# Kernel optimization log

Hardware: AMD Instinct MI355X
Metric: run time of the kernel (lower is better)

## Reference

```python
import jax, jax.numpy as jnp
import numpy as np

B, TIN, SOUT = 128, 256, 32
IN_DIM, H, L = 512, 512, 2
OUT_DIM = 100
D3 = 3 * OUT_DIM          # decoder effective out_dim (gt_type == 'tmc')
CAT = D3 + H              # 812, input dim of attn linears


def setup_inputs() -> dict:
    key = jax.random.key(0)
    ks = jax.random.split(key, 20)
    g = lambda k, s: jax.random.normal(k, s, dtype=jnp.float32) * 0.02
    return {
        "x": jax.random.normal(ks[0], (B, TIN, IN_DIM), dtype=jnp.float32),
        "target": jax.random.normal(ks[1], (B, SOUT + 1, OUT_DIM, 3), dtype=jnp.float32),
        # encoder GRU (num_layers=2, layer inputs are both 512-dim so weights stack)
        "enc_Wih": g(ks[2], (L, 3 * H, IN_DIM)),
        "enc_Whh": g(ks[3], (L, 3 * H, H)),
        "enc_bih": g(ks[4], (L, 3 * H)),
        "enc_bhh": g(ks[5], (L, 3 * H)),
        # decoder GRU (layer0 input = D3=300, layer1 input = H=512)
        "dec_Wih0": g(ks[6], (3 * H, D3)),
        "dec_Wih1": g(ks[7], (3 * H, H)),
        "dec_Whh": g(ks[8], (L, 3 * H, H)),
        "dec_bih": g(ks[9], (L, 3 * H)),
        "dec_bhh": g(ks[10], (L, 3 * H)),
        # attention linears
        "attnW_w": g(ks[11], (TIN, CAT)), "attnW_b": g(ks[12], (TIN,)),
        "attnC_w": g(ks[13], (D3, CAT)), "attnC_b": g(ks[14], (D3,)),
        # output MLP
        "out1_w": g(ks[15], (D3, H)), "out1_b": g(ks[16], (D3,)),
        "out2_w": g(ks[17], (D3, D3)), "out2_b": g(ks[18], (D3,)),
    }


def gru_cell(x, h, Wih, Whh, bih, bhh):
    """PyTorch-convention GRU cell. x:(B,Din) h:(B,H) -> (B,H)."""
    gi = x @ Wih.T + bih
    gh = h @ Whh.T + bhh
    ir, iz, inn = jnp.split(gi, 3, axis=-1)
    hr, hz, hn = jnp.split(gh, 3, axis=-1)
    r = jax.nn.sigmoid(ir + hr)
    z = jax.nn.sigmoid(iz + hz)
    n = jnp.tanh(inn + r * hn)
    return (1.0 - z) * n + z * h


def reference(x, target, enc_Wih, enc_Whh, enc_bih, enc_bhh,
              dec_Wih0, dec_Wih1, dec_Whh, dec_bih, dec_bhh,
              attnW_w, attnW_b, attnC_w, attnC_b,
              out1_w, out1_b, out2_w, out2_b):
    # ---- encoder: 2-layer GRU over time, zero initial hidden ----
    seq = jnp.transpose(x, (1, 0, 2))  # (T, B, D)
    hs = []
    for l in range(L):
        def step(h, xt, l=l):
            h2 = gru_cell(xt, h, enc_Wih[l], enc_Whh[l], enc_bih[l], enc_bhh[l])
            return h2, h2
        hT, seq = jax.lax.scan(step, jnp.zeros((B, H), x.dtype), seq)
        hs.append(hT)
    enc_out = jnp.transpose(seq, (1, 0, 2))      # (B, TIN, H)
    enc_hidden = jnp.stack(hs)                   # (L, B, H)

    # ---- decoder with teacher forcing (teacher_forcing_ratio=1.0) ----
    tgt = target[..., :3].reshape(B, SOUT + 1, D3)   # (B, SOUT+1, 300)
    xs = jnp.transpose(tgt[:, :SOUT, :], (1, 0, 2))  # (SOUT, B, 300)

    def dec_step(hidden, xt):
        cat = jnp.concatenate([xt, hidden[-1]], axis=-1)          # (B, 812)
        aw = jax.nn.softmax(cat @ attnW_w.T + attnW_b, axis=-1)   # (B, TIN)
        wctx = jnp.einsum('bt,bth->bh', aw, enc_out)              # (B, H)
        xc = jax.nn.relu(jnp.concatenate([xt, wctx], axis=-1) @ attnC_w.T + attnC_b)  # (B, 300)
        h0 = gru_cell(xc, hidden[0], dec_Wih0, dec_Whh[0], dec_bih[0], dec_bhh[0])
        h1 = gru_cell(h0, hidden[1], dec_Wih1, dec_Whh[1], dec_bih[1], dec_bhh[1])
        o = (h1 @ out1_w.T + out1_b) @ out2_w.T + out2_b          # (B, 300)
        return jnp.stack([h0, h1]), (o, aw)

    dec_hidden, (outs, aws) = jax.lax.scan(dec_step, enc_hidden, xs)
    dec_out = jnp.transpose(outs, (1, 0, 2))       # (B, SOUT, 300)
    attn_weights = jnp.transpose(aws, (1, 0, 2))   # (B, SOUT, TIN)
    return dec_out, dec_hidden, attn_weights
```

## Files before the change

kernel.cpp:

```cpp
#include <hip/hip_runtime.h>
#include <hip/hip_bf16.h>
#include <math.h>


#define NWG 128
#define TPB 256

typedef unsigned short u16;
typedef unsigned int   u32;
typedef short v8s __attribute__((ext_vector_type(8)));
typedef float v4f __attribute__((ext_vector_type(4)));

#define MFMA_(a,b,c) __builtin_amdgcn_mfma_f32_16x16x32_bf16((a),(b),(c),0,0,0)

__device__ __forceinline__ u16 f2bf(float f){
  unsigned u = __builtin_bit_cast(unsigned, f);
  unsigned r = u + 0x7FFFu + ((u >> 16) & 1u);
  return (u16)(r >> 16);
}
__device__ __forceinline__ float bf2f(u16 s){
  unsigned u = ((unsigned)s) << 16;
  return __builtin_bit_cast(float, u);
}
__device__ __forceinline__ void splitstore(u16* ph, u16* pl, float v){
  u16 h = f2bf(v); ph[0] = h; pl[0] = f2bf(v - bf2f(h));
}
__device__ __forceinline__ float sigm(float x){ return 1.f / (1.f + __expf(-x)); }
__device__ __forceinline__ float tanh_f(float x){
  float ax = fabsf(x);
  float t = __expf(-2.f * ax);
  float r = (1.f - t) / (1.f + t);
  return copysignf(r, x);
}

__device__ __forceinline__ v8s ldfrag(const u16* base, size_t ld, int r0, int k0){
  int lane = threadIdx.x & 63;
  const u16* p = base + (size_t)(r0 + (lane & 15)) * ld + (size_t)(k0 + ((lane >> 4) << 3));
  return *(const v8s*)p;
}

__device__ __forceinline__ void ldx4x4_sc0(v8s&o0,v8s&o1,v8s&o2,v8s&o3,
    const u16*p0,const u16*p1,const u16*p2,const u16*p3){
  asm volatile(
    "global_load_dwordx4 %0, %4, off sc0\n\t"
    "global_load_dwordx4 %1, %5, off sc0\n\t"
    "global_load_dwordx4 %2, %6, off sc0\n\t"
    "global_load_dwordx4 %3, %7, off sc0\n\t"
    "s_waitcnt vmcnt(0)"
    : "=&v"(o0),"=&v"(o1),"=&v"(o2),"=&v"(o3)
    : "v"(p0),"v"(p1),"v"(p2),"v"(p3) : "memory");
}
__device__ __forceinline__ void ldus4_sc0(u32&o0,u32&o1,u32&o2,u32&o3,
    const u16*p0,const u16*p1,const u16*p2,const u16*p3){
  asm volatile(
    "global_load_ushort %0, %4, off sc0\n\t"
    "global_load_ushort %1, %5, off sc0\n\t"
    "global_load_ushort %2, %6, off sc0\n\t"
    "global_load_ushort %3, %7, off sc0\n\t"
    "s_waitcnt vmcnt(0)"
    : "=&v"(o0),"=&v"(o1),"=&v"(o2),"=&v"(o3)
    : "v"(p0),"v"(p1),"v"(p2),"v"(p3) : "memory");
}

__device__ __forceinline__ v8s ldfrag_w(const u16* wlds, int gate, int kt){
  int lane = threadIdx.x & 63;
  int rr = lane & 15;
  int ch = (kt*4 + (lane >> 4)) ^ (rr & 7);
  return *(const v8s*)(wlds + (size_t)((gate*16 + rr)*64 + ch) * 8);
}
__device__ void stage_wslice(const float* Wf, u16* wlds, int col0){
  for (int idx = threadIdx.x; idx < 3*16*64; idx += TPB){
    int ch = idx & 63, rr = (idx >> 6) & 15, g = idx >> 10;
    const float* src = Wf + ((size_t)(g*512 + col0 + rr))*512 + ch*8;
    v4f f0 = *(const v4f*)src, f1 = *(const v4f*)(src + 4);
    v8s o;
    #pragma unroll
    for (int j=0;j<4;j++){ o[j] = (short)f2bf(f0[j]); o[4+j] = (short)f2bf(f1[j]); }
    *(v8s*)(wlds + (size_t)((g*16 + rr)*64 + (ch ^ (rr & 7))) * 8) = o;
  }
}
__device__ void stage_wslice_u16(const u16* Wh, const u16* Wl, u16* dh, u16* dl, int col0){
  for (int idx = threadIdx.x; idx < 3*16*64; idx += TPB){
    int ch = idx & 63, rr = (idx >> 6) & 15, g = idx >> 10;
    size_t so = ((size_t)(g*512 + col0 + rr))*512 + ch*8;
    size_t o  = (size_t)((g*16 + rr)*64 + (ch ^ (rr & 7))) * 8;
    *(v8s*)(dh+o) = *(const v8s*)(Wh+so);
    *(v8s*)(dl+o) = *(const v8s*)(Wl+so);
  }
}

struct KArgs {
  const float *x, *target, *eWih_f, *eWhh_f, *ebih, *ebhh;
  const float *dWih0_f, *dWih1_f, *dWhh_f, *dbih, *dbhh;
  const float *aWw_f, *aWb, *aCw_f, *aCb, *o1w_f, *o1b, *o2w_f, *o2b;
  float* out;
  u32 *flags, *genp, *ecnt, *lctr;
  u16 *ebf, *ehh;
  u16 *xhi, *h0hi, *h1hi, *encout;
  u16 *dWih0h,*dWih0l,*dWih1h,*dWih1l,*dWhhh,*dWhhl;
  u16 *Wwhh,*Wwhl,*Wwxh,*Wwxl,*Wchh,*Wchl,*Wcxh,*Wcxl;
  u16 *o2wh,*o2wl,*o1Th,*o1Tl,*Wph,*Wpl;
  float *bpr;
  u16 *xth,*xtl;
  float *preW,*preC;
  u16 *dh0h,*dh0l,*dh1h,*dh1l;
  float *logits;
  u16 *wcth,*wctl,*xch,*xcl;
};

__device__ __forceinline__ u32 ldcp(const u32* p){
  u32 r;
  asm volatile("global_load_dword %0, %1, off sc0 sc1\n\ts_waitcnt vmcnt(0)"
               : "=&v"(r) : "v"(p) : "memory");
  return r;
}

__device__ void gbar(u32* flags, u32* genp, u32 target){
  __syncthreads();
  int wg = blockIdx.x, tid = threadIdx.x;
  if (wg == 0){
    if (tid > 0 && tid < NWG){
      while (ldcp(&flags[tid]) < target) __builtin_amdgcn_s_sleep(1);
    }
    __syncthreads();
    if (tid == 0)
      __hip_atomic_fetch_add(genp, 1u, __ATOMIC_RELEASE, __HIP_MEMORY_SCOPE_AGENT);
  } else {
    if (tid == 0){
      __hip_atomic_fetch_add(&flags[wg], 1u, __ATOMIC_RELEASE, __HIP_MEMORY_SCOPE_AGENT);
      while (ldcp(genp) < target) __builtin_amdgcn_s_sleep(1);
    }
  }
  __builtin_amdgcn_fence(__ATOMIC_ACQUIRE, "agent");
  __syncthreads();
}

__device__ void lbar(u32* ctr, u32 target){
  __syncthreads();
  if (threadIdx.x == 0){
    __hip_atomic_fetch_add(ctr, 1u, __ATOMIC_RELAXED, __HIP_MEMORY_SCOPE_AGENT);
    while (ldcp(ctr) < target) __builtin_amdgcn_s_sleep(1);
  }
  __syncthreads();
}

__device__ __forceinline__ v4f tile_xwT(const u16* Ah, const u16* Al, size_t lda, int nks,
                                        const u16* Bh, const u16* Bl, size_t ldb,
                                        int row0, int brow0, v4f* red){
  int tid = threadIdx.x, w = tid >> 6, lane = tid & 63;
  v4f acc[4];
  #pragma unroll
  for (int i=0;i<4;i++) acc[i] = (v4f){0.f,0.f,0.f,0.f};
  for (int ks = w; ks < nks; ks += 4){
    int k0 = ks * 32;
    v8s bh = ldfrag(Bh, ldb, brow0, k0);
    v8s bl = ldfrag(Bl, ldb, brow0, k0);
    #pragma unroll
    for (int rt=0; rt<4; rt++){
      v8s a  = ldfrag(Ah, lda, row0 + rt*16, k0);
      v8s al = ldfrag(Al, lda, row0 + rt*16, k0);
      acc[rt] = MFMA_(a,  bh, acc[rt]);
      acc[rt] = MFMA_(al, bh, acc[rt]);
      acc[rt] = MFMA_(a,  bl, acc[rt]);
    }
  }
  __syncthreads();
  red[(0*4+w)*64+lane]=acc[0]; red[(1*4+w)*64+lane]=acc[1];
  red[(2*4+w)*64+lane]=acc[2]; red[(3*4+w)*64+lane]=acc[3];
  __syncthreads();
  v4f g = red[(w*4+0)*64+lane];
  g += red[(w*4+1)*64+lane]; g += red[(w*4+2)*64+lane]; g += red[(w*4+3)*64+lane];
  return g;
}

__device__ __forceinline__ void gru_tile_pin(const u16* Axh, const u16* Axl, size_t ldx, int nkx,
                                             const u16* Ahh, const u16* Ahl,
                                             const u16* Wi,  const u16* Wil, size_t ldwi,
                                             const u16* whp, const u16* wlp,
                                             int row0, int col0, v4f* red, v4f* gate){
  int tid = threadIdx.x, w = tid >> 6, lane = tid & 63;
  v4f acc[4][4];
  #pragma unroll
  for (int i=0;i<4;i++){
    #pragma unroll
    for (int j=0;j<4;j++) acc[i][j] = (v4f){0.f,0.f,0.f,0.f};
  }
  for (int ks = w; ks < nkx; ks += 4){
    int k0 = ks * 32;
    v8s br = ldfrag(Wi, ldwi,        col0, k0);
    v8s bz = ldfrag(Wi, ldwi,  512 + col0, k0);
    v8s bn = ldfrag(Wi, ldwi, 1024 + col0, k0);
    v8s brl = ldfrag(Wil, ldwi, col0, k0);
    v8s bzl = ldfrag(Wil, ldwi, 512+col0, k0);
    v8s bnl = ldfrag(Wil, ldwi, 1024+col0, k0);
    #pragma unroll
    for (int rt=0; rt<4; rt++){
      v8s a  = ldfrag(Axh, ldx, row0 + rt*16, k0);
      v8s al = ldfrag(Axl, ldx, row0 + rt*16, k0);
      acc[rt][0] = MFMA_(a, br, acc[rt][0]); acc[rt][0] = MFMA_(al, br, acc[rt][0]); acc[rt][0] = MFMA_(a, brl, acc[rt][0]);
      acc[rt][1] = MFMA_(a, bz, acc[rt][1]); acc[rt][1] = MFMA_(al, bz, acc[rt][1]); acc[rt][1] = MFMA_(a, bzl, acc[rt][1]);
      acc[rt][2] = MFMA_(a, bn, acc[rt][2]); acc[rt][2] = MFMA_(al, bn, acc[rt][2]); acc[rt][2] = MFMA_(a, bnl, acc[rt][2]);
    }
  }
  for (int ks = w; ks < 16; ks += 4){
    int k0 = ks * 32;
    v8s br  = ldfrag_w(whp, 0, ks), bz  = ldfrag_w(whp, 1, ks), bn  = ldfrag_w(whp, 2, ks);
    v8s brl = ldfrag_w(wlp, 0, ks), bzl = ldfrag_w(wlp, 1, ks), bnl = ldfrag_w(wlp, 2, ks);
    #pragma unroll
    for (int rt=0; rt<4; rt++){
      v8s a  = ldfrag(Ahh, 512, row0 + rt*16, k0);
      v8s al = ldfrag(Ahl, 512, row0 + rt*16, k0);
      acc[rt][0] = MFMA_(a, br, acc[rt][0]); acc[rt][0] = MFMA_(al, br, acc[rt][0]); acc[rt][0] = MFMA_(a, brl, acc[rt][0]);
      acc[rt][1] = MFMA_(a, bz, acc[rt][1]); acc[rt][1] = MFMA_(al, bz, acc[rt][1]); acc[rt][1] = MFMA_(a, bzl, acc[rt][1]);
      acc[rt][3] = MFMA_(a, bn, acc[rt][3]); acc[rt][3] = MFMA_(al, bn, acc[rt][3]); acc[rt][3] = MFMA_(a, bnl, acc[rt][3]);
    }
  }
  #pragma unroll
  for (int ty=0; ty<4; ty++){
    __syncthreads();
    red[(0*4+w)*64+lane]=acc[0][ty]; red[(1*4+w)*64+lane]=acc[1][ty];
    red[(2*4+w)*64+lane]=acc[2][ty]; red[(3*4+w)*64+lane]=acc[3][ty];
    __syncthreads();
    v4f g = red[(w*4+0)*64+lane];
    g += red[(w*4+1)*64+lane]; g += red[(w*4+2)*64+lane]; g += red[(w*4+3)*64+lane];
    gate[ty] = g;
  }
}

__device__ __forceinline__ void gru_combine(const v4f* gate, const float* bih, const float* bhh,
                                            const u16* Hph, const u16* Hpl,
                                            u16* Hnh, u16* Hnl,
                                            int row0, int col0){
  int tid = threadIdx.x, w = tid >> 6, lane = tid & 63;
  int col  = col0 + (lane & 15);
  int rowb = row0 + w*16 + ((lane >> 4) << 2);
  float bir = bih[col], biz = bih[512+col], bin = bih[1024+col];
  float bhr = bhh[col], bhz = bhh[512+col], bhn = bhh[1024+col];
  #pragma unroll
  for (int e=0; e<4; e++){
    int row = rowb + e;
    float r = sigm(gate[0][e] + bir + bhr);
    float z = sigm(gate[1][e] + biz + bhz);
    float n = tanh_f(gate[2][e] + bin + r * (gate[3][e] + bhn));
    float hp = bf2f(Hph[(size_t)row*512 + col]) + bf2f(Hpl[(size_t)row*512 + col]);
    float hv = (1.f - z) * n + z * hp;
    splitstore(&Hnh[(size_t)row*512+col], &Hnl[(size_t)row*512+col], hv);
  }
}

__device__ void enc_step3(const u16* Xb, size_t ldX, const u16* Hp, u16* Hn,
                          u16* encw, int t, const u16* wI, const u16* wH,
                          const float* bih, const float* bhh, int col0, int row0){
  const int tid = threadIdx.x, w = tid>>6, lane = tid&63;
  v4f aR=(v4f){0,0,0,0}, aZ=aR, aNI=aR, aNH=aR;
  const int r0 = row0 + w*16;
  for (int kt=0; kt<16; ++kt){
    int k0 = kt*32;
    v8s bi0=ldfrag_w(wI,0,kt), bi1=ldfrag_w(wI,1,kt), bi2=ldfrag_w(wI,2,kt);
    v8s bh0=ldfrag_w(wH,0,kt), bh1=ldfrag_w(wH,1,kt), bh2=ldfrag_w(wH,2,kt);
    v8s ax = ldfrag(Xb, ldX, r0, k0);
    v8s ah = ldfrag(Hp, 512, r0, k0);
    aR=MFMA_(ax,bi0,aR); aZ=MFMA_(ax,bi1,aZ); aNI=MFMA_(ax,bi2,aNI);
    aR=MFMA_(ah,bh0,aR); aZ=MFMA_(ah,bh1,aZ); aNH=MFMA_(ah,bh2,aNH);
  }
  int col = col0 + (lane&15);
  float bir=bih[col], biz=bih[512+col], bin=bih[1024+col];
  float bhr=bhh[col], bhz=bhh[512+col], bhn=bhh[1024+col];
  int rowb = r0 + ((lane>>4)<<2);
  #pragma unroll
  for (int e=0;e<4;e++){
    int row = rowb + e;
    float r = sigm(aR[e] + bir + bhr);
    float z = sigm(aZ[e] + biz + bhz);
    float n = tanh_f(aNI[e] + bin + r*(aNH[e] + bhn));
    float hp = bf2f(Hp[(size_t)row*512 + col]);
    float hv = (1.f-z)*n + z*hp;
    u16 h16 = f2bf(hv);
    Hn[(size_t)row*512 + col] = h16;
    if (encw) encw[((size_t)row*256 + t)*512 + col] = h16;
  }
}

__device__ void enc_stepL(const u16* Xb, size_t ldX, int xsc0,
                          const u16* Hp, u16* Hn, u16* encw, int t,
                          const u16* Wih, const u16* Whh,
                          const float* bih, const float* bhh,
                          int b0, int c0, v4f* red){
  const int tid = threadIdx.x, w = tid>>6, lane = tid&63;
  v4f acc[2][4];
  #pragma unroll
  for (int i=0;i<2;i++)
    #pragma unroll
    for (int j=0;j<4;j++) acc[i][j] = (v4f){0,0,0,0};
  const size_t lo = (size_t)((lane>>4)<<3);
  v8s ax0,ax1,ax2,ax3, ah0,ah1,ah2,ah3;
  {
    const u16* hrow = Hp + (size_t)(b0 + (lane&15))*512 + lo;
    ldx4x4_sc0(ah0,ah1,ah2,ah3,
               hrow + (w*4+0)*32, hrow + (w*4+1)*32, hrow + (w*4+2)*32, hrow + (w*4+3)*32);
  }
  if (xsc0){
    const u16* xrow = Xb + (size_t)(lane&15)*ldX + lo;
    ldx4x4_sc0(ax0,ax1,ax2,ax3,
               xrow + (w*4+0)*32, xrow + (w*4+1)*32, xrow + (w*4+2)*32, xrow + (w*4+3)*32);
  } else {
    ax0 = ldfrag(Xb, ldX, 0, (w*4+0)*32);
    ax1 = ldfrag(Xb, ldX, 0, (w*4+1)*32);
    ax2 = ldfrag(Xb, ldX, 0, (w*4+2)*32);
    ax3 = ldfrag(Xb, ldX, 0, (w*4+3)*32);
  }
  v8s axs[4] = {ax0,ax1,ax2,ax3};
  v8s ahs[4] = {ah0,ah1,ah2,ah3};
  #pragma unroll
  for (int j=0;j<4;j++){
    int k0 = (w*4+j)*32;
    #pragma unroll
    for (int ct=0; ct<2; ct++){
      int cc = c0 + ct*16;
      acc[ct][0] = MFMA_(axs[j], ldfrag(Wih,512,cc,k0),      acc[ct][0]);
      acc[ct][1] = MFMA_(axs[j], ldfrag(Wih,512,512+cc,k0),  acc[ct][1]);
      acc[ct][2] = MFMA_(axs[j], ldfrag(Wih,512,1024+cc,k0), acc[ct][2]);
      acc[ct][0] = MFMA_(ahs[j], ldfrag(Whh,512,cc,k0),      acc[ct][0]);
      acc[ct][1] = MFMA_(ahs[j], ldfrag(Whh,512,512+cc,k0),  acc[ct][1]);
      acc[ct][3] = MFMA_(ahs[j], ldfrag(Whh,512,1024+cc,k0), acc[ct][3]);
    }
  }
  __syncthreads();
  #pragma unroll
  for (int ct=0; ct<2; ct++)
    #pragma unroll
    for (int g=0; g<4; g++)
      red[((ct*4+g)*4 + w)*64 + lane] = acc[ct][g];
  __syncthreads();
  if (w < 2){
    v4f gate[4];
    #pragma unroll
    for (int g=0; g<4; g++){
      v4f s = red[((w*4+g)*4+0)*64+lane];
      s += red[((w*4+g)*4+1)*64+lane];
      s += red[((w*4+g)*4+2)*64+lane];
      s += red[((w*4+g)*4+3)*64+lane];
      gate[g] = s;
    }
    int col = c0 + w*16 + (lane&15);
    int lb  = ((lane>>4)<<2);
    u32 hp0,hp1,hp2,hp3;
    ldus4_sc0(hp0,hp1,hp2,hp3,
              Hp + (size_t)(b0+lb+0)*512 + col, Hp + (size_t)(b0+lb+1)*512 + col,
              Hp + (size_t)(b0+lb+2)*512 + col, Hp + (size_t)(b0+lb+3)*512 + col);
    u32 hpv[4] = {hp0,hp1,hp2,hp3};
    float bir=bih[col], biz=bih[512+col], bin=bih[1024+col];
    float bhr=bhh[col], bhz=bhh[512+col], bhn=bhh[1024+col];
    #pragma unroll
    for (int e=0;e<4;e++){
      int row = b0 + lb + e;
      float r = sigm(gate[0][e] + bir + bhr);
      float z = sigm(gate[1][e] + biz + bhz);
      float n = tanh_f(gate[2][e] + bin + r*(gate[3][e] + bhn));
      float hv = (1.f-z)*n + z*bf2f((u16)hpv[e]);
      u16 h16 = f2bf(hv);
      Hn[(size_t)row*512 + col] = h16;
      if (encw) encw[((size_t)row*256 + t)*512 + col] = h16;
    }
  }
}

__device__ __forceinline__ float blk_max(float v, float* sred){
  #pragma unroll
  for (int off=32; off>0; off>>=1) v = fmaxf(v, __shfl_xor(v, off, 64));
  __syncthreads();
  if ((threadIdx.x & 63) == 0) sred[threadIdx.x >> 6] = v;
  __syncthreads();
  return fmaxf(fmaxf(sred[0], sred[1]), fmaxf(sred[2], sred[3]));
}
__device__ __forceinline__ float blk_sum(float v, float* sred){
  #pragma unroll
  for (int off=32; off>0; off>>=1) v += __shfl_xor(v, off, 64);
  __syncthreads();
  if ((threadIdx.x & 63) == 0) sred[threadIdx.x >> 6] = v;
  __syncthreads();
  return sred[0] + sred[1] + sred[2] + sred[3];
}

#define DECOUT_OFF 0
#define DECHID_OFF 1228800
#define ATTN_OFF   1359872

__global__ void __launch_bounds__(TPB, 1) traffic_kernel(KArgs A){
  __shared__ struct { u16 wI[3*16*64*8]; u16 wH[3*16*64*8]; } WL;
  __shared__ v4f red[8*4*64];
  __shared__ float sred[4];
  __shared__ float awl2[256];
  __shared__ int sh_xcd, sh_slot, sh_bal;
  const int tid = threadIdx.x;
  const int wg  = blockIdx.x;
  const size_t gtid = (size_t)wg * TPB + tid;
  const size_t P = (size_t)NWG * TPB;
  u32 bt = 0;

  {
    u32 xcd;
    asm volatile("s_getreg_b32 %0, hwreg(HW_REG_XCC_ID)" : "=s"(xcd));
    if (tid == 0){
      sh_xcd = (int)(xcd & 7);
      sh_slot = (int)__hip_atomic_fetch_add(&A.ecnt[sh_xcd], 1u, __ATOMIC_RELAXED, __HIP_MEMORY_SCOPE_AGENT);
    }
    __syncthreads();
  }

  for (size_t i=gtid; i<128UL*256*512; i+=P) A.xhi[i] = f2bf(A.x[i]);
  for (size_t i=gtid; i<2UL*1536*512; i+=P){ A.ebf[i]=f2bf(A.eWih_f[i]); A.ehh[i]=f2bf(A.eWhh_f[i]); }
  for (size_t i=gtid; i<1536UL*320; i+=P){
    size_t r=i/320, c=i%320;
    float v = (c<300)? A.dWih0_f[r*300+c] : 0.f;
    splitstore(&A.dWih0h[i], &A.dWih0l[i], v);
  }
  for (size_t i=gtid; i<1536UL*512; i+=P) splitstore(&A.dWih1h[i], &A.dWih1l[i], A.dWih1_f[i]);
  for (size_t i=gtid; i<2UL*1536*512; i+=P) splitstore(&A.dWhhh[i], &A.dWhhl[i], A.dWhh_f[i]);
  for (size_t i=gtid; i<256UL*512; i+=P){ size_t r=i>>9, c=i&511; splitstore(&A.Wwhh[i], &A.Wwhl[i], A.aWw_f[r*812+300+c]); }
  for (size_t i=gtid; i<256UL*320; i+=P){ size_t r=i/320, c=i%320; float v=(c<300)? A.aWw_f[r*812+c]:0.f; splitstore(&A.Wwxh[i], &A.Wwxl[i], v); }
  for (size_t i=gtid; i<304UL*512; i+=P){ size_t r=i>>9, c=i&511; float v=(r<300)? A.aCw_f[r*812+300+c]:0.f; splitstore(&A.Wchh[i], &A.Wchl[i], v); }
  for (size_t i=gtid; i<304UL*320; i+=P){ size_t r=i/320, c=i%320; float v=(r<300&&c<300)? A.aCw_f[r*812+c]:0.f; splitstore(&A.Wcxh[i], &A.Wcxl[i], v); }
  for (size_t i=gtid; i<320UL*320; i+=P){ size_t r=i/320, c=i%320; float v=(r<300&&c<300)? A.o2w_f[r*300+c]:0.f; splitstore(&A.o2wh[i], &A.o2wl[i], v); }
  for (size_t i=gtid; i<512UL*320; i+=P){
    size_t j=i/320, k=i%320;
    float v = (k<300)? A.o1w_f[k*512+j] : 0.f;
    splitstore(&A.o1Th[i], &A.o1Tl[i], v);
  }
  for (size_t i=gtid; i<304; i+=P){
    float s = 0.f;
    if (i < 300){
      s = A.o2b[i];
      const float* wrow = A.o2w_f + i*300;
      for (int k=0;k<300;k++) s += wrow[k] * A.o1b[k];
    }
    A.bpr[i] = s;
  }
  for (size_t i=gtid; i<32UL*128*320; i+=P){
    size_t sb=i/320, c=i%320, s2=sb>>7, b=sb&127;
    float v = (c<300)? A.target[(b*33+s2)*300 + c] : 0.f;
    splitstore(&A.xth[i], &A.xtl[i], v);
  }
  for (size_t i=gtid; i<65536; i+=P){ A.h0hi[i]=0; A.h1hi[i]=0; }
  for (size_t i=gtid; i<128UL*320; i+=P){ A.xch[i]=0; A.xcl[i]=0; }
  gbar(A.flags, A.genp, ++bt);

  if (tid == 0){
    int ok = 1;
    for (int x2=0; x2<8; x2++)
      ok &= (__hip_atomic_fetch_add(&A.ecnt[x2], 0u, __ATOMIC_RELAXED, __HIP_MEMORY_SCOPE_AGENT) == 16u);
    sh_bal = ok;
  }
  __syncthreads();
  const int vwg = sh_bal ? (sh_xcd*16 + sh_slot) : wg;

  for (int tl = vwg; tl < 1024; tl += NWG){
    int rb = tl >> 4, cb = tl & 15;
    int row0 = rb*64, col0 = cb*16;
    v4f g = tile_xwT(A.xth, A.xtl, 320, 10, A.Wwxh, A.Wwxl, 320, row0, col0, red);
    int w = tid>>6, lane = tid&63;
    int col = col0 + (lane&15), rowb = row0 + w*16 + ((lane>>4)<<2);
    #pragma unroll
    for (int e=0;e<4;e++){ int row=rowb+e; A.preW[(size_t)row*256+col] = g[e] + A.aWb[col]; }
  }
  for (int tl = vwg; tl < 1216; tl += NWG){
    int rb = tl / 19, cb = tl % 19;
    int row0 = rb*64, col0 = cb*16;
    v4f g = tile_xwT(A.xth, A.xtl, 320, 10, A.Wcxh, A.Wcxl, 320, row0, col0, red);
    int w = tid>>6, lane = tid&63;
    int col = col0 + (lane&15), rowb = row0 + w*16 + ((lane>>4)<<2);
    #pragma unroll
    for (int e=0;e<4;e++){
      int row=rowb+e;
      float v = (col<300)? (g[e] + A.aCb[col]) : 0.f;
      A.preC[(size_t)row*320+col] = v;
    }
  }
  for (int tl = vwg; tl < 160; tl += NWG){
    int rt = tl >> 5, ct = tl & 31;
    int row0 = rt*64, col0 = ct*16;
    v4f g = tile_xwT(A.o2wh, A.o2wl, 320, 10, A.o1Th, A.o1Tl, 320, row0, col0, red);
    int w = tid>>6, lane = tid&63;
    int col = col0 + (lane&15), rowb = row0 + w*16 + ((lane>>4)<<2);
    #pragma unroll
    for (int e=0;e<4;e++){
      int row = rowb+e;
      if (row < 304) splitstore(&A.Wph[(size_t)row*512+col], &A.Wpl[(size_t)row*512+col], g[e]);
    }
  }
  gbar(A.flags, A.genp, ++bt);

  if (sh_bal){
    const int b0 = sh_xcd*16, c0 = sh_slot*32;
    u32* ctr = A.lctr + sh_xcd*16;
    u32 lt = 0;
    for (int t=0; t<256; ++t){
      enc_stepL(A.xhi + (size_t)b0*131072 + (size_t)t*512, 131072, 0,
                A.h0hi + (size_t)t*65536, A.h0hi + (size_t)(t+1)*65536,
                nullptr, 0, A.ebf, A.ehh, A.ebih, A.ebhh, b0, c0, red);
      lbar(ctr, 16u*(++lt));
    }
    const u16* W1i = A.ebf + (size_t)1536*512;
    const u16* W1h = A.ehh + (size_t)1536*512;
    for (int t=0; t<256; ++t){
      enc_stepL(A.h0hi + (size_t)(t+1)*65536 + (size_t)b0*512, 512, 1,
                A.h1hi + (size_t)(t&1)*65536, A.h1hi + (size_t)((t+1)&1)*65536,
                A.encout, t, W1i, W1h, A.ebih + 1536, A.ebhh + 1536, b0, c0, red);
      lbar(ctr, 16u*(++lt));
    }
  } else {
    const int grp  = vwg >> 6;
    const int half = (vwg >> 5) & 1;
    const int col0 = (vwg & 31) * 16;
    const int row0 = half * 64;
    stage_wslice(A.eWih_f + (size_t)grp*1536*512, WL.wI, col0);
    stage_wslice(A.eWhh_f + (size_t)grp*1536*512, WL.wH, col0);
    __syncthreads();
    const float* bih = A.ebih + grp*1536;
    const float* bhh = A.ebhh + grp*1536;
    for (int k=0; k<=256; ++k){
      if (grp == 0){
        if (k < 256)
          enc_step3(A.xhi + (size_t)k*512, (size_t)256*512,
                    A.h0hi + (size_t)k*65536, A.h0hi + (size_t)(k+1)*65536,
                    nullptr, 0, WL.wI, WL.wH, bih, bhh, col0, row0);
      } else {
        if (k >= 1){
          int t = k-1;
          enc_step3(A.h0hi + (size_t)k*65536, 512,
                    A.h1hi + (size_t)(t&1)*65536, A.h1hi + (size_t)((t+1)&1)*65536,
                    A.encout, t, WL.wI, WL.wH, bih, bhh, col0, row0);
        }
      }
      gbar(A.flags, A.genp, ++bt);
    }
  }
  gbar(A.flags, A.genp, ++bt);

  for (size_t i=gtid; i<65536; i+=P){
    A.dh0h[i] = A.h0hi[(size_t)256*65536 + i]; A.dh0l[i] = 0;
    A.dh1h[i] = A.h1hi[i];                     A.dh1l[i] = 0;
  }
  if (vwg < 64){
    int cb = vwg & 31;
    stage_wslice_u16(A.dWhhh, A.dWhhl, WL.wI, WL.wH, cb*16);
  } else {
    int cb = (vwg - 64) & 31;
    stage_wslice_u16(A.dWhhh + (size_t)1536*512, A.dWhhl + (size_t)1536*512, WL.wI, WL.wH, cb*16);
  }
  gbar(A.flags, A.genp, ++bt);

  for (int s=0; s<32; s++){
    const u16* h0ph = A.dh0h + (size_t)(s&1)*65536;
    const u16* h0pl = A.dh0l + (size_t)(s&1)*65536;
    u16* h0nh = A.dh0h + (size_t)((s+1)&1)*65536;
    u16* h0nl = A.dh0l + (size_t)((s+1)&1)*65536;
    const u16* h1ph = A.dh1h + (size_t)(s&1)*65536;
    const u16* h1pl = A.dh1l + (size_t)(s&1)*65536;
    u16* h1nh = A.dh1h + (size_t)((s+1)&1)*65536;
    u16* h1nl = A.dh1l + (size_t)((s+1)&1)*65536;

    if (vwg < 32){
      int rb = vwg >> 4, cb = vwg & 15;
      int row0 = rb*64, col0 = cb*16;
      v4f g = tile_xwT(h1ph, h1pl, 512, 16, A.Wwhh, A.Wwhl, 512, row0, col0, red);
      const float* pre = A.preW + (size_t)s*128*256;
      int w = tid>>6, lane = tid&63;
      int col = col0 + (lane&15), rowb = row0 + w*16 + ((lane>>4)<<2);
      #pragma unroll
      for (int e=0;e<4;e++){ int row=rowb+e; A.logits[(size_t)row*256+col] = g[e] + pre[(size_t)row*256+col]; }
    } else if (vwg >= 64 && vwg < 102 && s > 0){
      int v2 = vwg - 64;
      int rb = v2 / 19, cb = v2 % 19;
      int row0 = rb*64, col0 = cb*16;
      v4f g = tile_xwT(h1ph, h1pl, 512, 16, A.Wph, A.Wpl, 512, row0, col0, red);
      int w = tid>>6, lane = tid&63;
      int col = col0 + (lane&15), rowb = row0 + w*16 + ((lane>>4)<<2);
      #pragma unroll
      for (int e=0;e<4;e++){
        int row = rowb+e;
        if (col < 300) A.out[DECOUT_OFF + ((size_t)row*32 + (s-1))*300 + col] = g[e] + A.bpr[col];
      }
    }
    gbar(A.flags, A.genp, ++bt);

    {
      int b = vwg;
      float v = A.logits[(size_t)b*256 + tid];
      float m = blk_max(v, sred);
      float e = __expf(v - m);
      float ssum = blk_sum(e, sred);
      float awv = e / ssum;
      awl2[tid] = awv;
      A.out[ATTN_OFF + ((size_t)b*32 + s)*256 + tid] = awv;
      __syncthreads();
      int w4 = tid >> 6, lane = tid & 63;
      const u16* ebase = A.encout + (size_t)b*256*512 + (size_t)(w4*64)*512 + lane*8;
      float acc8[8];
      #pragma unroll
      for (int q=0;q<8;q++) acc8[q]=0.f;
      for (int j=0;j<64;++j){
        float wv = awl2[w4*64+j];
        v8s ev = *(const v8s*)(ebase + (size_t)j*512);
        #pragma unroll
        for (int q=0;q<8;q++) acc8[q] += wv * bf2f((u16)ev[q]);
      }
      float* rr = (float*)red;
      #pragma unroll
      for (int q=0;q<8;q++) rr[(size_t)tid*8+q] = acc8[q];
      __syncthreads();
      #pragma unroll
      for (int cc=0; cc<2; ++cc){
        int col = tid*2+cc;
        float sum = 0.f;
        #pragma unroll
        for (int w2=0; w2<4; ++w2) sum += rr[(((size_t)w2*64 + (col>>3))<<3) + (col&7)];
        splitstore(&A.wcth[(size_t)b*512+col], &A.wctl[(size_t)b*512+col], sum);
      }
    }
    gbar(A.flags, A.genp, ++bt);

    if (vwg < 38){
      int rb = vwg / 19, cb = vwg % 19;
      int row0 = rb*64, col0 = cb*16;
      v4f g = tile_xwT(A.wcth, A.wctl, 512, 16, A.Wchh, A.Wchl, 512, row0, col0, red);
      const float* pre = A.preC + (size_t)s*128*320;
      int w = tid>>6, lane = tid&63;
      int col = col0 + (lane&15), rowb = row0 + w*16 + ((lane>>4)<<2);
      #pragma unroll
      for (int e=0;e<4;e++){
        int row = rowb+e;
        float v = (col<300)? fmaxf(g[e] + pre[(size_t)row*320+col], 0.f) : 0.f;
        splitstore(&A.xch[(size_t)row*320+col], &A.xcl[(size_t)row*320+col], v);
      }
    }
    gbar(A.flags, A.genp, ++bt);

    if (vwg < 64){
      int rb = vwg >> 5, cb = vwg & 31;
      int row0 = rb*64, col0 = cb*16;
      v4f gate[4];
      gru_tile_pin(A.xch, A.xcl, 320, 10, h0ph, h0pl,
                   A.dWih0h, A.dWih0l, 320, WL.wI, WL.wH, row0, col0, red, gate);
      gru_combine(gate, A.dbih, A.dbhh, h0ph, h0pl, h0nh, h0nl, row0, col0);
    }
    gbar(A.flags, A.genp, ++bt);

    if (vwg >= 64){
      int v2 = vwg - 64;
      int rb = v2 >> 5, cb = v2 & 31;
      int row0 = rb*64, col0 = cb*16;
      v4f gate[4];
      gru_tile_pin(h0nh, h0nl, 512, 16, h1ph, h1pl,
                   A.dWih1h, A.dWih1l, 512, WL.wI, WL.wH, row0, col0, red, gate);
      gru_combine(gate, A.dbih + 1536, A.dbhh + 1536, h1ph, h1pl, h1nh, h1nl, row0, col0);
    }
    gbar(A.flags, A.genp, ++bt);
  }

  if (vwg >= 64 && vwg < 102){
    int v2 = vwg - 64;
    int rb = v2 / 19, cb = v2 % 19;
    int row0 = rb*64, col0 = cb*16;
    v4f g = tile_xwT(A.dh1h, A.dh1l, 512, 16, A.Wph, A.Wpl, 512, row0, col0, red);
    int w = tid>>6, lane = tid&63;
    int col = col0 + (lane&15), rowb = row0 + w*16 + ((lane>>4)<<2);
    #pragma unroll
    for (int e=0;e<4;e++){
      int row = rowb+e;
      if (col < 300) A.out[DECOUT_OFF + ((size_t)row*32 + 31)*300 + col] = g[e] + A.bpr[col];
    }
  }

  for (size_t i=gtid; i<65536; i+=P){
    A.out[DECHID_OFF + i]         = bf2f(A.dh0h[i]) + bf2f(A.dh0l[i]);
    A.out[DECHID_OFF + 65536 + i] = bf2f(A.dh1h[i]) + bf2f(A.dh1l[i]);
  }
}

extern "C" void kernel_launch(void* const* d_in, const int* in_sizes, int n_in,
                              void* d_out, int out_size, void* d_ws, size_t ws_size,
                              hipStream_t stream){
  (void)in_sizes; (void)n_in; (void)out_size; (void)ws_size;
  KArgs A;
  A.x       = (const float*)d_in[0];  A.target = (const float*)d_in[1];
  A.eWih_f  = (const float*)d_in[2];  A.eWhh_f = (const float*)d_in[3];
  A.ebih    = (const float*)d_in[4];  A.ebhh   = (const float*)d_in[5];
  A.dWih0_f = (const float*)d_in[6];  A.dWih1_f= (const float*)d_in[7];
  A.dWhh_f  = (const float*)d_in[8];  A.dbih   = (const float*)d_in[9];
  A.dbhh    = (const float*)d_in[10];
  A.aWw_f   = (const float*)d_in[11]; A.aWb    = (const float*)d_in[12];
  A.aCw_f   = (const float*)d_in[13]; A.aCb    = (const float*)d_in[14];
  A.o1w_f   = (const float*)d_in[15]; A.o1b    = (const float*)d_in[16];
  A.o2w_f   = (const float*)d_in[17]; A.o2b    = (const float*)d_in[18];
  A.out = (float*)d_out;

  char* w = (char*)d_ws;
  size_t off = 0;
  auto alloc = [&](size_t bytes)->char*{
    char* p = w + off; off += (bytes + 255) & ~(size_t)255; return p;
  };
  char* barp = alloc(4096);
  A.flags  = (u32*)barp;
  A.genp   = (u32*)(barp + 2048);
  A.ecnt   = (u32*)(barp + 2304);
  A.lctr   = (u32*)(barp + 2560);
  A.ebf    = (u16*)alloc(2UL*1536*512*2);
  A.ehh    = (u16*)alloc(2UL*1536*512*2);
  A.xhi    = (u16*)alloc(128UL*256*512*2);
  A.h0hi   = (u16*)alloc(257UL*128*512*2);
  A.h1hi   = (u16*)alloc(2UL*128*512*2);
  A.encout = A.xhi;
  A.dWih0h = (u16*)alloc(1536UL*320*2); A.dWih0l = (u16*)alloc(1536UL*320*2);
  A.dWih1h = (u16*)alloc(1536UL*512*2); A.dWih1l = (u16*)alloc(1536UL*512*2);
  A.dWhhh  = (u16*)alloc(2UL*1536*512*2); A.dWhhl = (u16*)alloc(2UL*1536*512*2);
  A.Wwhh   = (u16*)alloc(256UL*512*2);  A.Wwhl   = (u16*)alloc(256UL*512*2);
  A.Wwxh   = (u16*)alloc(256UL*320*2);  A.Wwxl   = (u16*)alloc(256UL*320*2);
  A.Wchh   = (u16*)alloc(304UL*512*2);  A.Wchl   = (u16*)alloc(304UL*512*2);
  A.Wcxh   = (u16*)alloc(304UL*320*2);  A.Wcxl   = (u16*)alloc(304UL*320*2);
  A.o2wh   = (u16*)alloc(320UL*320*2);  A.o2wl   = (u16*)alloc(320UL*320*2);
  A.o1Th   = (u16*)alloc(512UL*320*2);  A.o1Tl   = (u16*)alloc(512UL*320*2);
  A.Wph    = (u16*)alloc(304UL*512*2);  A.Wpl    = (u16*)alloc(304UL*512*2);
  A.bpr    = (float*)alloc(304UL*4);
  A.xth    = (u16*)alloc(32UL*128*320*2); A.xtl  = (u16*)alloc(32UL*128*320*2);
  A.preW   = (float*)alloc(32UL*128*256*4);
  A.preC   = (float*)alloc(32UL*128*320*4);
  A.dh0h   = (u16*)alloc(2UL*65536*2); A.dh0l = (u16*)alloc(2UL*65536*2);
  A.dh1h   = (u16*)alloc(2UL*65536*2); A.dh1l = (u16*)alloc(2UL*65536*2);
  A.logits = (float*)alloc(128UL*256*4);
  A.wcth   = (u16*)alloc(128UL*512*2); A.wctl = (u16*)alloc(128UL*512*2);
  A.xch    = (u16*)alloc(128UL*320*2); A.xcl  = (u16*)alloc(128UL*320*2);

  hipMemsetAsync(d_ws, 0, 4096, stream);
  traffic_kernel<<<dim3(NWG), dim3(TPB), 0, stream>>>(A);
}
```

Measured before the change: 7.792 ms.

## Replace atomic barriers with padded flag-store barriers and XCD-local L2 polling

```diff
diff --git a/kernel.cpp b/kernel.cpp
--- a/kernel.cpp
+++ b/kernel.cpp
@@ -94,7 +94,7 @@
   const float *dWih0_f, *dWih1_f, *dWhh_f, *dbih, *dbhh;
   const float *aWw_f, *aWb, *aCw_f, *aCb, *o1w_f, *o1b, *o2w_f, *o2b;
   float* out;
-  u32 *flags, *genp, *ecnt, *lctr;
+  u32 *flags, *genp, *ecnt, *lflags, *lgen;
   u16 *ebf, *ehh;
   u16 *xhi, *h0hi, *h1hi, *encout;
   u16 *dWih0h,*dWih0l,*dWih1h,*dWih1l,*dWhhh,*dWhhl;
@@ -114,20 +114,36 @@
                : "=&v"(r) : "v"(p) : "memory");
   return r;
 }
-
-__device__ void gbar(u32* flags, u32* genp, u32 target){
-  __syncthreads();
+__device__ __forceinline__ void stcp(u32* p, u32 v){
+  asm volatile("global_store_dword %0, %1, off sc0 sc1" :: "v"(p), "v"(v) : "memory");
+}
+__device__ __forceinline__ u32 ldl(const u32* p, u32 it){
+  u32 r;
+  if ((it & 63u) != 0u)
+    asm volatile("global_load_dword %0, %1, off sc0\n\ts_waitcnt vmcnt(0)"
+                 : "=&v"(r) : "v"(p) : "memory");
+  else
+    asm volatile("global_load_dword %0, %1, off sc0 sc1\n\ts_waitcnt vmcnt(0)"
+                 : "=&v"(r) : "v"(p) : "memory");
+  return r;
+}
+__device__ __forceinline__ void stl(u32* p, u32 v){
+  asm volatile("global_store_dword %0, %1, off sc0" :: "v"(p), "v"(v) : "memory");
+}
+
+__device__ void gbarF(u32* flags, u32* genp, u32 target){
+  __syncthreads();
+  __builtin_amdgcn_fence(__ATOMIC_RELEASE, "agent");
   int wg = blockIdx.x, tid = threadIdx.x;
   if (wg == 0){
     if (tid > 0 && tid < NWG){
-      while (ldcp(&flags[tid]) < target) __builtin_amdgcn_s_sleep(1);
+      while (ldcp(flags + (size_t)tid*16) < target) __builtin_amdgcn_s_sleep(1);
     }
     __syncthreads();
-    if (tid == 0)
-      __hip_atomic_fetch_add(genp, 1u, __ATOMIC_RELEASE, __HIP_MEMORY_SCOPE_AGENT);
+    if (tid == 0) stcp(genp, target);
   } else {
     if (tid == 0){
-      __hip_atomic_fetch_add(&flags[wg], 1u, __ATOMIC_RELEASE, __HIP_MEMORY_SCOPE_AGENT);
+      stcp(flags + (size_t)wg*16, target);
       while (ldcp(genp) < target) __builtin_amdgcn_s_sleep(1);
     }
   }
@@ -135,11 +151,23 @@
   __syncthreads();
 }
 
-__device__ void lbar(u32* ctr, u32 target){
-  __syncthreads();
-  if (threadIdx.x == 0){
-    __hip_atomic_fetch_add(ctr, 1u, __ATOMIC_RELAXED, __HIP_MEMORY_SCOPE_AGENT);
-    while (ldcp(ctr) < target) __builtin_amdgcn_s_sleep(1);
+__device__ void lbarF(u32* lflags, u32* lgen, int slot, u32 target){
+  asm volatile("s_waitcnt vmcnt(0)" ::: "memory");
+  __syncthreads();
+  int tid = threadIdx.x;
+  if (slot == 0){
+    if (tid >= 1 && tid < 16){
+      u32 it = 0;
+      while (ldl(lflags + (size_t)tid*16, ++it) < target) __builtin_amdgcn_s_sleep(1);
+    }
+    __syncthreads();
+    if (tid == 0) stl(lgen, target);
+  } else {
+    if (tid == 0){
+      stl(lflags + (size_t)slot*16, target);
+      u32 it = 0;
+      while (ldl(lgen, ++it) < target) __builtin_amdgcn_s_sleep(1);
+    }
   }
   __syncthreads();
 }
@@ -403,7 +431,8 @@
     asm volatile("s_getreg_b32 %0, hwreg(HW_REG_XCC_ID)" : "=s"(xcd));
     if (tid == 0){
       sh_xcd = (int)(xcd & 7);
-      sh_slot = (int)__hip_atomic_fetch_add(&A.ecnt[sh_xcd], 1u, __ATOMIC_RELAXED, __HIP_MEMORY_SCOPE_AGENT);
+      sh_slot = (int)__hip_atomic_fetch_add(A.ecnt + (size_t)(xcd & 7)*16, 1u,
+                                            __ATOMIC_RELAXED, __HIP_MEMORY_SCOPE_AGENT);
     }
     __syncthreads();
   }
@@ -443,12 +472,12 @@
   }
   for (size_t i=gtid; i<65536; i+=P){ A.h0hi[i]=0; A.h1hi[i]=0; }
   for (size_t i=gtid; i<128UL*320; i+=P){ A.xch[i]=0; A.xcl[i]=0; }
-  gbar(A.flags, A.genp, ++bt);
+  gbarF(A.flags, A.genp, ++bt);
 
   if (tid == 0){
     int ok = 1;
     for (int x2=0; x2<8; x2++)
-      ok &= (__hip_atomic_fetch_add(&A.ecnt[x2], 0u, __ATOMIC_RELAXED, __HIP_MEMORY_SCOPE_AGENT) == 16u);
+      ok &= (ldcp(A.ecnt + (size_t)x2*16) == 16u);
     sh_bal = ok;
   }
   __syncthreads();
@@ -488,17 +517,18 @@
       if (row < 304) splitstore(&A.Wph[(size_t)row*512+col], &A.Wpl[(size_t)row*512+col], g[e]);
     }
   }
-  gbar(A.flags, A.genp, ++bt);
+  gbarF(A.flags, A.genp, ++bt);
 
   if (sh_bal){
     const int b0 = sh_xcd*16, c0 = sh_slot*32;
-    u32* ctr = A.lctr + sh_xcd*16;
+    u32* lfl = A.lflags + (size_t)sh_xcd*256;
+    u32* lgn = A.lgen   + (size_t)sh_xcd*16;
     u32 lt = 0;
     for (int t=0; t<256; ++t){
       enc_stepL(A.xhi + (size_t)b0*131072 + (size_t)t*512, 131072, 0,
                 A.h0hi + (size_t)t*65536, A.h0hi + (size_t)(t+1)*65536,
                 nullptr, 0, A.ebf, A.ehh, A.ebih, A.ebhh, b0, c0, red);
-      lbar(ctr, 16u*(++lt));
+      lbarF(lfl, lgn, sh_slot, ++lt);
     }
     const u16* W1i = A.ebf + (size_t)1536*512;
     const u16* W1h = A.ehh + (size_t)1536*512;
@@ -506,7 +536,7 @@
       enc_stepL(A.h0hi + (size_t)(t+1)*65536 + (size_t)b0*512, 512, 1,
                 A.h1hi + (size_t)(t&1)*65536, A.h1hi + (size_t)((t+1)&1)*65536,
                 A.encout, t, W1i, W1h, A.ebih + 1536, A.ebhh + 1536, b0, c0, red);
-      lbar(ctr, 16u*(++lt));
+      lbarF(lfl, lgn, sh_slot, ++lt);
     }
   } else {
     const int grp  = vwg >> 6;
@@ -532,10 +562,10 @@
                     A.encout, t, WL.wI, WL.wH, bih, bhh, col0, row0);
         }
       }
-      gbar(A.flags, A.genp, ++bt);
-    }
-  }
-  gbar(A.flags, A.genp, ++bt);
+      gbarF(A.flags, A.genp, ++bt);
+    }
+  }
+  gbarF(A.flags, A.genp, ++bt);
 
   for (size_t i=gtid; i<65536; i+=P){
     A.dh0h[i] = A.h0hi[(size_t)256*65536 + i]; A.dh0l[i] = 0;
@@ -548,7 +578,7 @@
     int cb = (vwg - 64) & 31;
     stage_wslice_u16(A.dWhhh + (size_t)1536*512, A.dWhhl + (size_t)1536*512, WL.wI, WL.wH, cb*16);
   }
-  gbar(A.flags, A.genp, ++bt);
+  gbarF(A.flags, A.genp, ++bt);
 
   for (int s=0; s<32; s++){
     const u16* h0ph = A.dh0h + (size_t)(s&1)*65536;
@@ -582,7 +612,7 @@
         if (col < 300) A.out[DECOUT_OFF + ((size_t)row*32 + (s-1))*300 + col] = g[e] + A.bpr[col];
       }
     }
-    gbar(A.flags, A.genp, ++bt);
+    gbarF(A.flags, A.genp, ++bt);
 
     {
       int b = vwg;
@@ -618,7 +648,7 @@
         splitstore(&A.wcth[(size_t)b*512+col], &A.wctl[(size_t)b*512+col], sum);
       }
     }
-    gbar(A.flags, A.genp, ++bt);
+    gbarF(A.flags, A.genp, ++bt);
 
     if (vwg < 38){
       int rb = vwg / 19, cb = vwg % 19;
@@ -634,7 +664,7 @@
         splitstore(&A.xch[(size_t)row*320+col], &A.xcl[(size_t)row*320+col], v);
       }
     }
-    gbar(A.flags, A.genp, ++bt);
+    gbarF(A.flags, A.genp, ++bt);
 
     if (vwg < 64){
       int rb = vwg >> 5, cb = vwg & 31;
@@ -644,7 +674,7 @@
                    A.dWih0h, A.dWih0l, 320, WL.wI, WL.wH, row0, col0, red, gate);
       gru_combine(gate, A.dbih, A.dbhh, h0ph, h0pl, h0nh, h0nl, row0, col0);
     }
-    gbar(A.flags, A.genp, ++bt);
+    gbarF(A.flags, A.genp, ++bt);
 
     if (vwg >= 64){
       int v2 = vwg - 64;
@@ -655,7 +685,7 @@
                    A.dWih1h, A.dWih1l, 512, WL.wI, WL.wH, row0, col0, red, gate);
       gru_combine(gate, A.dbih + 1536, A.dbhh + 1536, h1ph, h1pl, h1nh, h1nl, row0, col0);
     }
-    gbar(A.flags, A.genp, ++bt);
+    gbarF(A.flags, A.genp, ++bt);
   }
 
   if (vwg >= 64 && vwg < 102){
@@ -700,11 +730,12 @@
   auto alloc = [&](size_t bytes)->char*{
     char* p = w + off; off += (bytes + 255) & ~(size_t)255; return p;
   };
-  char* barp = alloc(4096);
+  char* barp = alloc(32768);
   A.flags  = (u32*)barp;
-  A.genp   = (u32*)(barp + 2048);
-  A.ecnt   = (u32*)(barp + 2304);
-  A.lctr   = (u32*)(barp + 2560);
+  A.genp   = (u32*)(barp + 8192);
+  A.ecnt   = (u32*)(barp + 8448);
+  A.lflags = (u32*)(barp + 9472);
+  A.lgen   = (u32*)(barp + 17664);
   A.ebf    = (u16*)alloc(2UL*1536*512*2);
   A.ehh    = (u16*)alloc(2UL*1536*512*2);
   A.xhi    = (u16*)alloc(128UL*256*512*2);
@@ -731,6 +762,6 @@
   A.wcth   = (u16*)alloc(128UL*512*2); A.wctl = (u16*)alloc(128UL*512*2);
   A.xch    = (u16*)alloc(128UL*320*2); A.xcl  = (u16*)alloc(128UL*320*2);
 
-  hipMemsetAsync(d_ws, 0, 4096, stream);
+  hipMemsetAsync(d_ws, 0, 32768, stream);
   traffic_kernel<<<dim3(NWG), dim3(TPB), 0, stream>>>(A);
 }
```

Measured after the change: 12.40 ms. 1.59x slower.
